# Kernel tuning notes

Hardware: AMD Instinct MI355X
Metric: run time of the kernel (lower is better)

Reference implementation:

```python
import jax, jax.numpy as jnp
import numpy as np

ALPHA = 1.702
EPS_RMS = 1e-6
W_LOAD = 0.01
W_IMP = 0.01
W_AUX = 1.0
LIMIT = 7.0
K_TOP = 4


def swiglu(x, alpha=ALPHA, limit=LIMIT):
    x_glu = jnp.clip(x[..., ::2], -limit, limit)
    x_lin = jnp.clip(x[..., 1::2], -limit, limit)
    return x_glu * jax.nn.sigmoid(x_glu * alpha) + (x_lin + 1.0)


def setup_inputs() -> dict:
    key = jax.random.key(0)
    ks = jax.random.split(key, 4)
    T, H, I, E = 2048, 512, 512, 8
    x = jax.random.normal(ks[0], (T, H), dtype=jnp.float32)
    norm_scale = jnp.ones((H,), jnp.float32)
    gate_w = jax.random.normal(ks[1], (E, H), jnp.float32) * 0.02
    gate_b = jnp.zeros((E,), jnp.float32)
    mlp1_w = jax.random.normal(ks[2], (E, 2 * I, H), jnp.float32) * 0.02
    mlp1_b = jnp.zeros((E, 2 * I), jnp.float32)
    mlp2_w = jax.random.normal(ks[3], (E, H, I), jnp.float32) * 0.02
    mlp2_b = jnp.zeros((E, H), jnp.float32)
    return {"x": x, "norm_scale": norm_scale, "gate_w": gate_w, "gate_b": gate_b,
            "mlp1_w": mlp1_w, "mlp1_b": mlp1_b, "mlp2_w": mlp2_w, "mlp2_b": mlp2_b}


def reference(x, norm_scale, gate_w, gate_b, mlp1_w, mlp1_b, mlp2_w, mlp2_b):
    T, H = x.shape
    E = gate_w.shape[0]
    K = K_TOP
    # RMSNorm (fp32 math as in torch module)
    t = x * jax.lax.rsqrt(jnp.mean(x * x, axis=-1, keepdims=True) + EPS_RMS) * norm_scale
    # gating
    gate_logits = t @ gate_w.T + gate_b                      # [T, E]
    gate_probs = jax.nn.softmax(gate_logits, axis=-1)
    expert_weights, experts_indices = jax.lax.top_k(gate_probs, K)
    expert_weights = expert_weights / expert_weights.sum(axis=-1, keepdims=True)
    # per-token per-expert combine coefficient (sum of slot weights routed to e)
    coeff = jnp.zeros((T, E), x.dtype).at[jnp.arange(T)[:, None], experts_indices].add(expert_weights)
    # dense expert compute (math-equivalent to the gathered einsums; avoids
    # materializing per-token weight matrices)
    h = jnp.einsum('th,ech->tec', t, mlp1_w) + mlp1_b[None]  # [T, E, 2I]
    a = swiglu(h)                                            # [T, E, I]
    y = jnp.einsum('tei,ehi->teh', a, mlp2_w) + mlp2_b[None] # [T, E, H]
    out = jnp.einsum('teh,te->th', y, coeff) + x
    # aux losses (replicates the torch code exactly, incl. D-doubling quirk)
    P = gate_probs.mean(axis=0)                              # [E]
    counts = jax.vmap(lambda col: jnp.zeros((E,), x.dtype).at[col].add(1.0), in_axes=1)(experts_indices)  # [K, E]
    doubling = (2.0 ** (K - jnp.arange(K))).astype(x.dtype)  # D_i = 2*(D_{i-1}+c_i)
    D = (doubling[:, None] * counts).sum(axis=0) / (T * K)
    loss_load = W_LOAD * E * (P * D).sum()
    importance = gate_logits.sum(axis=0)
    cv = jnp.std(importance, ddof=1) / (importance.mean() + 1e-6)
    loss_imp = W_IMP * cv ** 2
    aux_loss = W_AUX * (loss_load + loss_imp)
    return out, aux_loss
```

## Files before the change

kernel.cpp:

```cpp
#include <hip/hip_runtime.h>
#include <stdint.h>

#define ALPHA 1.702f
#define LIMIT 7.0f

typedef float f32x4 __attribute__((ext_vector_type(4)));
typedef __bf16 bf16x8 __attribute__((ext_vector_type(8)));

static __device__ __forceinline__ unsigned short f2bf(float f) {
    union { float f; uint32_t u; } v; v.f = f;
    uint32_t u = v.u;
    return (unsigned short)((u + 0x7FFFu + ((u >> 16) & 1u)) >> 16);
}
static __device__ __forceinline__ int imin(int a, int b) { return a < b ? a : b; }

#define GLL16(GP, LP) __builtin_amdgcn_global_load_lds( \
    (const __attribute__((address_space(1))) void*)(GP), \
    (__attribute__((address_space(3))) void*)(LP), 16, 0, 0)

static __device__ __forceinline__ int lsw(int row, int kc) {
    return row * 4 + (kc ^ ((row >> 1) & 3));
}

__global__ __launch_bounds__(256) void prep_kernel(
    const float* __restrict__ w1, const float* __restrict__ w2,
    unsigned short* __restrict__ w1p, unsigned short* __restrict__ w2b,
    const float* __restrict__ x,
    const float* __restrict__ norm_scale,
    const float* __restrict__ gate_w,
    const float* __restrict__ gate_b,
    const float* __restrict__ b2,
    unsigned short* __restrict__ t_bf,
    int* __restrict__ idx,
    float* __restrict__ wcoef,
    int* __restrict__ cnt,
    float* __restrict__ paux,
    float* __restrict__ out)
{
    __shared__ float red[4][48];
    __shared__ int   ltok[8][8];
    __shared__ float lwt[8][8];
    __shared__ int   lcnt[8];
    __shared__ int   gbase[8];
    if (blockIdx.x < 6144) {
        const int i4 = blockIdx.x * 256 + threadIdx.x;
        const int n1 = 1048576;
        if (i4 < n1) {
            const int e = i4 >> 17;
            const int rem = i4 & 131071;
            const int r = rem >> 7;
            const int c = rem & 127;
            const int src = (r < 512) ? (2 * r) : (2 * (r - 512) + 1);
            float4 v = ((const float4*)w1)[(e << 17) + (src << 7) + c];
            ushort4 o = { f2bf(v.x), f2bf(v.y), f2bf(v.z), f2bf(v.w) };
            ((ushort4*)w1p)[i4] = o;
        } else {
            const int i2 = i4 - n1;
            float4 v = ((const float4*)w2)[i2];
            ushort4 o = { f2bf(v.x), f2bf(v.y), f2bf(v.z), f2bf(v.w) };
            ((ushort4*)w2b)[i2] = o;
        }
        return;
    }
    const int bid = blockIdx.x - 6144;
    const int wave = threadIdx.x >> 6;
    const int lane = threadIdx.x & 63;
    if (threadIdx.x < 8) lcnt[threadIdx.x] = 0;
    __syncthreads();

    float accP[8], accI[8], accC[32];
    #pragma unroll
    for (int e = 0; e < 8; ++e) { accP[e] = 0.f; accI[e] = 0.f; }
    #pragma unroll
    for (int i = 0; i < 32; ++i) accC[i] = 0.f;

    #pragma unroll
    for (int it = 0; it < 2; ++it) {
        const int t = bid * 8 + wave * 2 + it;
        const float4* xr = (const float4*)(x + t * 512);
        float4 x0 = xr[lane * 2];
        float4 x1 = xr[lane * 2 + 1];
        float ss = x0.x*x0.x + x0.y*x0.y + x0.z*x0.z + x0.w*x0.w
                 + x1.x*x1.x + x1.y*x1.y + x1.z*x1.z + x1.w*x1.w;
        #pragma unroll
        for (int off = 32; off > 0; off >>= 1) ss += __shfl_xor(ss, off, 64);
        const float rstd = rsqrtf(ss * (1.f / 512.f) + 1e-6f);
        const float4* sr = (const float4*)norm_scale;
        float4 s0 = sr[lane * 2], s1 = sr[lane * 2 + 1];
        float tv[8];
        tv[0] = x0.x * rstd * s0.x; tv[1] = x0.y * rstd * s0.y;
        tv[2] = x0.z * rstd * s0.z; tv[3] = x0.w * rstd * s0.w;
        tv[4] = x1.x * rstd * s1.x; tv[5] = x1.y * rstd * s1.y;
        tv[6] = x1.z * rstd * s1.z; tv[7] = x1.w * rstd * s1.w;
        uint32_t p0 = (uint32_t)f2bf(tv[0]) | ((uint32_t)f2bf(tv[1]) << 16);
        uint32_t p1 = (uint32_t)f2bf(tv[2]) | ((uint32_t)f2bf(tv[3]) << 16);
        uint32_t p2 = (uint32_t)f2bf(tv[4]) | ((uint32_t)f2bf(tv[5]) << 16);
        uint32_t p3 = (uint32_t)f2bf(tv[6]) | ((uint32_t)f2bf(tv[7]) << 16);
        uint4 pk; pk.x = p0; pk.y = p1; pk.z = p2; pk.w = p3;
        ((uint4*)(t_bf + t * 512))[lane] = pk;
        float le[8];
        #pragma unroll
        for (int e = 0; e < 8; ++e) {
            const float4* gw = (const float4*)(gate_w + e * 512);
            float4 g0 = gw[lane * 2], g1 = gw[lane * 2 + 1];
            float d = tv[0]*g0.x + tv[1]*g0.y + tv[2]*g0.z + tv[3]*g0.w
                    + tv[4]*g1.x + tv[5]*g1.y + tv[6]*g1.z + tv[7]*g1.w;
            #pragma unroll
            for (int off = 32; off > 0; off >>= 1) d += __shfl_xor(d, off, 64);
            le[e] = d + gate_b[e];
        }
        float mx = le[0];
        #pragma unroll
        for (int e = 1; e < 8; ++e) mx = fmaxf(mx, le[e]);
        float pe[8], se = 0.f;
        #pragma unroll
        for (int e = 0; e < 8; ++e) { pe[e] = __expf(le[e] - mx); se += pe[e]; }
        const float sinv = 1.f / se;
        #pragma unroll
        for (int e = 0; e < 8; ++e) pe[e] *= sinv;
        unsigned picked = 0;
        int ik[4]; float wk[4];
        #pragma unroll
        for (int k = 0; k < 4; ++k) {
            float bv = -1.f; int bi = 0;
            #pragma unroll
            for (int e = 0; e < 8; ++e)
                if (!(picked & (1u << e)) && pe[e] > bv) { bv = pe[e]; bi = e; }
            ik[k] = bi; wk[k] = bv; picked |= (1u << bi);
        }
        const float winv = 1.f / (wk[0] + wk[1] + wk[2] + wk[3]);
        float nw[4];
        #pragma unroll
        for (int k = 0; k < 4; ++k) nw[k] = wk[k] * winv;
        float ce[8];
        #pragma unroll
        for (int e = 0; e < 8; ++e) {
            float c = 0.f;
            #pragma unroll
            for (int k = 0; k < 4; ++k) c += (ik[k] == e) ? nw[k] : 0.f;
            ce[e] = c;
        }
        if (lane == 0) {
            #pragma unroll
            for (int k = 0; k < 4; ++k) {
                const int e = ik[k];
                const int pos = atomicAdd(&lcnt[e], 1);
                ltok[e][pos] = t; lwt[e][pos] = nw[k];
            }
        }
        #pragma unroll
        for (int e = 0; e < 8; ++e) { accP[e] += pe[e]; accI[e] += le[e]; }
        #pragma unroll
        for (int k = 0; k < 4; ++k)
            #pragma unroll
            for (int e = 0; e < 8; ++e)
                accC[k * 8 + e] += (ik[k] == e) ? 1.f : 0.f;
        float ov[8];
        ov[0] = x0.x; ov[1] = x0.y; ov[2] = x0.z; ov[3] = x0.w;
        ov[4] = x1.x; ov[5] = x1.y; ov[6] = x1.z; ov[7] = x1.w;
        #pragma unroll
        for (int e = 0; e < 8; ++e) {
            const float4* br = (const float4*)(b2 + e * 512);
            float4 b0 = br[lane * 2], bb1 = br[lane * 2 + 1];
            ov[0] += ce[e] * b0.x; ov[1] += ce[e] * b0.y;
            ov[2] += ce[e] * b0.z; ov[3] += ce[e] * b0.w;
            ov[4] += ce[e] * bb1.x; ov[5] += ce[e] * bb1.y;
            ov[6] += ce[e] * bb1.z; ov[7] += ce[e] * bb1.w;
        }
        float4 o0, o1;
        o0.x = ov[0]; o0.y = ov[1]; o0.z = ov[2]; o0.w = ov[3];
        o1.x = ov[4]; o1.y = ov[5]; o1.z = ov[6]; o1.w = ov[7];
        float4* orow = (float4*)(out + t * 512);
        orow[lane * 2] = o0; orow[lane * 2 + 1] = o1;
    }
    if (lane == 0) {
        #pragma unroll
        for (int e = 0; e < 8; ++e) { red[wave][e] = accP[e]; red[wave][8 + e] = accI[e]; }
        #pragma unroll
        for (int i = 0; i < 32; ++i) red[wave][16 + i] = accC[i];
    }
    __syncthreads();
    if (threadIdx.x < 8)
        gbase[threadIdx.x] = atomicAdd(&cnt[threadIdx.x], lcnt[threadIdx.x]);
    __syncthreads();
    if (threadIdx.x < 64) {
        const int e = threadIdx.x >> 3, i = threadIdx.x & 7;
        if (i < lcnt[e]) {
            const int g = gbase[e] + i;
            idx[e * 2048 + g] = ltok[e][i];
            wcoef[e * 2048 + g] = lwt[e][i];
        }
    }
    if (threadIdx.x < 48) {
        paux[bid * 48 + threadIdx.x] =
            red[0][threadIdx.x] + red[1][threadIdx.x]
          + red[2][threadIdx.x] + red[3][threadIdx.x];
    }
}

__global__ __launch_bounds__(256, 2) void gemm1_swiglu(
    const unsigned short* __restrict__ A,
    const unsigned short* __restrict__ w1p,
    const float* __restrict__ b1,
    const int* __restrict__ idx,
    const float* __restrict__ wcoef,
    const int* __restrict__ cnt,
    unsigned short* __restrict__ As,
    const float* __restrict__ paux,
    float* __restrict__ aux_out)
{
    if (blockIdx.x == 512) {
        __shared__ float sred[4][48];
        const int wv = threadIdx.x >> 6, ln = threadIdx.x & 63;
        if (ln < 48) {
            float s = 0.f;
            for (int b = 0; b < 64; ++b) s += paux[(wv * 64 + b) * 48 + ln];
            sred[wv][ln] = s;
        }
        __syncthreads();
        if (threadIdx.x == 0) {
            float imp[8], sl = 0.f;
            #pragma unroll
            for (int e = 0; e < 8; ++e) {
                float a0 = sred[0][e] + sred[1][e] + sred[2][e] + sred[3][e];
                float P = a0 * (1.f / 2048.f);
                imp[e] = sred[0][8+e] + sred[1][8+e] + sred[2][8+e] + sred[3][8+e];
                float c0 = sred[0][16+e] + sred[1][16+e] + sred[2][16+e] + sred[3][16+e];
                float c1 = sred[0][24+e] + sred[1][24+e] + sred[2][24+e] + sred[3][24+e];
                float c2 = sred[0][32+e] + sred[1][32+e] + sred[2][32+e] + sred[3][32+e];
                float c3 = sred[0][40+e] + sred[1][40+e] + sred[2][40+e] + sred[3][40+e];
                float D = (16.f * c0 + 8.f * c1 + 4.f * c2 + 2.f * c3) * (1.f / 8192.f);
                sl += P * D;
            }
            float loss_load = 0.01f * 8.f * sl;
            float mean = 0.f;
            #pragma unroll
            for (int e = 0; e < 8; ++e) mean += imp[e];
            mean *= 0.125f;
            float var = 0.f;
            #pragma unroll
            for (int e = 0; e < 8; ++e) { float d = imp[e] - mean; var += d * d; }
            var *= (1.f / 7.f);
            float cv = sqrtf(var) / (mean + 1e-6f);
            *aux_out = loss_load + 0.01f * cv * cv;
        }
        return;
    }
    const int bx = blockIdx.x;
    const int e = bx & 7;
    const int slot = bx >> 3;
    const int tile_m = slot >> 2, tile_n = slot & 3;
    const int m0 = tile_m * 128, np = tile_n * 128;
    const int cnte = cnt[e];
    if (m0 >= cnte) return;

    __shared__ unsigned short tA[2][4096];
    __shared__ unsigned short tBg[2][4096];
    __shared__ unsigned short tBl[2][4096];
    const int tid = threadIdx.x;
    const int lane = tid & 63, wave = tid >> 6;
    const int wm = (wave & 1) * 64, wn = (wave >> 1) * 64;
    const int quad = lane >> 4, l16 = lane & 15;
    const int srow = tid >> 2;
    const int soff = ((tid & 3) ^ ((tid >> 3) & 3)) * 8;

    const int tok0 = idx[e * 2048 + imin(m0 + srow, cnte - 1)];
    const int tok1 = idx[e * 2048 + imin(m0 + 64 + srow, cnte - 1)];
    const unsigned short* Ar0 = A + tok0 * 512 + soff;
    const unsigned short* Ar1 = A + tok1 * 512 + soff;
    const unsigned short* Bg = w1p + (e * 1024 + np) * 512;
    const unsigned short* Bg0 = Bg + srow * 512 + soff;
    const unsigned short* Bg1 = Bg + (64 + srow) * 512 + soff;
    const unsigned short* Bl0 = Bg0 + 512 * 512;
    const unsigned short* Bl1 = Bg1 + 512 * 512;

    int rA[4], rB[4];
    #pragma unroll
    for (int i = 0; i < 4; ++i) {
        rA[i] = lsw(wm + i * 16 + l16, quad) * 8;
        rB[i] = lsw(wn + i * 16 + l16, quad) * 8;
    }

    f32x4 accG[4][4], accL[4][4];
    #pragma unroll
    for (int i = 0; i < 4; ++i)
        #pragma unroll
        for (int j = 0; j < 4; ++j) {
            f32x4 z = {0.f, 0.f, 0.f, 0.f};
            accG[i][j] = z; accL[i][j] = z;
        }

#define STAGE1(s, k0) do { \
    GLL16(Ar0 + (k0), tA[s] + tid * 8); \
    GLL16(Ar1 + (k0), tA[s] + (tid + 256) * 8); \
    GLL16(Bg0 + (k0), tBg[s] + tid * 8); \
    GLL16(Bg1 + (k0), tBg[s] + (tid + 256) * 8); \
    GLL16(Bl0 + (k0), tBl[s] + tid * 8); \
    GLL16(Bl1 + (k0), tBl[s] + (tid + 256) * 8); \
} while (0)

    STAGE1(0, 0);
    STAGE1(1, 32);
    #pragma unroll
    for (int kt = 0; kt < 16; ++kt) {
        const int cur = kt & 1;
        if (kt < 15) asm volatile("s_waitcnt vmcnt(6)" ::: "memory");
        else         asm volatile("s_waitcnt vmcnt(0)" ::: "memory");
        asm volatile("s_barrier" ::: "memory");
        bf16x8 af[4], bg[4], bl[4];
        #pragma unroll
        for (int i = 0; i < 4; ++i) {
            af[i] = *(const bf16x8*)(tA[cur] + rA[i]);
            bg[i] = *(const bf16x8*)(tBg[cur] + rB[i]);
            bl[i] = *(const bf16x8*)(tBl[cur] + rB[i]);
        }
        asm volatile("s_waitcnt lgkmcnt(0)" ::: "memory");
        asm volatile("s_barrier" ::: "memory");
        if (kt < 14) STAGE1(cur, (kt + 2) * 32);
        #pragma unroll
        for (int i = 0; i < 4; ++i)
            #pragma unroll
            for (int j = 0; j < 4; ++j) {
                accG[i][j] = __builtin_amdgcn_mfma_f32_16x16x32_bf16(af[i], bg[j], accG[i][j], 0, 0, 0);
                accL[i][j] = __builtin_amdgcn_mfma_f32_16x16x32_bf16(af[i], bl[j], accL[i][j], 0, 0, 0);
            }
    }
#undef STAGE1

    #pragma unroll
    for (int j = 0; j < 4; ++j) {
        const int colp = np + wn + j * 16 + l16;
        const float bgv = b1[e * 1024 + 2 * colp];
        const float blv = b1[e * 1024 + 2 * colp + 1];
        #pragma unroll
        for (int i = 0; i < 4; ++i) {
            const int sb = m0 + wm + i * 16 + quad * 4;
            #pragma unroll
            for (int r = 0; r < 4; ++r) {
                const int s = sb + r;
                if (s < cnte) {
                    float g2 = fminf(fmaxf(accG[i][j][r] + bgv, -LIMIT), LIMIT);
                    float l2 = fminf(fmaxf(accL[i][j][r] + blv, -LIMIT), LIMIT);
                    float a = g2 / (1.f + __expf(-ALPHA * g2)) + l2 + 1.f;
                    a *= wcoef[e * 2048 + s];
                    As[e * 1048576 + s * 512 + colp] = f2bf(a);
                }
            }
        }
    }
}

__global__ __launch_bounds__(256, 2) void gemm2(
    const unsigned short* __restrict__ As,
    const unsigned short* __restrict__ w2b,
    const int* __restrict__ idx,
    const int* __restrict__ cnt,
    float* __restrict__ out)
{
    const int bx = blockIdx.x;
    const int e = bx & 7;
    const int slot = bx >> 3;
    const int tile_m = slot >> 2, tile_n = slot & 3;
    const int m0 = tile_m * 128, n0 = tile_n * 128;
    const int cnte = cnt[e];
    if (m0 >= cnte) return;

    __shared__ unsigned short tA[2][4096];
    __shared__ unsigned short tB[2][4096];
    const int tid = threadIdx.x;
    const int lane = tid & 63, wave = tid >> 6;
    const int wm = (wave & 1) * 64, wn = (wave >> 1) * 64;
    const int quad = lane >> 4, l16 = lane & 15;
    const int srow = tid >> 2;
    const int soff = ((tid & 3) ^ ((tid >> 3) & 3)) * 8;

    const unsigned short* Ar0 = As + e * 1048576 + (m0 + srow) * 512 + soff;
    const unsigned short* Ar1 = As + e * 1048576 + (m0 + 64 + srow) * 512 + soff;
    const unsigned short* Bb  = w2b + e * 262144;
    const unsigned short* Br0 = Bb + (n0 + srow) * 512 + soff;
    const unsigned short* Br1 = Bb + (n0 + 64 + srow) * 512 + soff;

    int rA[4], rB[4];
    #pragma unroll
    for (int i = 0; i < 4; ++i) {
        rA[i] = lsw(wm + i * 16 + l16, quad) * 8;
        rB[i] = lsw(wn + i * 16 + l16, quad) * 8;
    }

    f32x4 acc[4][4];
    #pragma unroll
    for (int i = 0; i < 4; ++i)
        #pragma unroll
        for (int j = 0; j < 4; ++j) { f32x4 z = {0.f, 0.f, 0.f, 0.f}; acc[i][j] = z; }

#define STAGE2(s, k0) do { \
    GLL16(Ar0 + (k0), tA[s] + tid * 8); \
    GLL16(Ar1 + (k0), tA[s] + (tid + 256) * 8); \
    GLL16(Br0 + (k0), tB[s] + tid * 8); \
    GLL16(Br1 + (k0), tB[s] + (tid + 256) * 8); \
} while (0)

    STAGE2(0, 0);
    STAGE2(1, 32);
    #pragma unroll
    for (int kt = 0; kt < 16; ++kt) {
        const int cur = kt & 1;
        if (kt < 15) asm volatile("s_waitcnt vmcnt(4)" ::: "memory");
        else         asm volatile("s_waitcnt vmcnt(0)" ::: "memory");
        asm volatile("s_barrier" ::: "memory");
        bf16x8 af[4], bf[4];
        #pragma unroll
        for (int i = 0; i < 4; ++i) {
            af[i] = *(const bf16x8*)(tA[cur] + rA[i]);
            bf[i] = *(const bf16x8*)(tB[cur] + rB[i]);
        }
        asm volatile("s_waitcnt lgkmcnt(0)" ::: "memory");
        asm volatile("s_barrier" ::: "memory");
        if (kt < 14) STAGE2(cur, (kt + 2) * 32);
        #pragma unroll
        for (int i = 0; i < 4; ++i)
            #pragma unroll
            for (int j = 0; j < 4; ++j)
                acc[i][j] = __builtin_amdgcn_mfma_f32_16x16x32_bf16(af[i], bf[j], acc[i][j], 0, 0, 0);
    }
#undef STAGE2

    #pragma unroll
    for (int i = 0; i < 4; ++i) {
        const int sb = m0 + wm + i * 16 + quad * 4;
        #pragma unroll
        for (int r = 0; r < 4; ++r) {
            const int s = sb + r;
            if (s < cnte) {
                const int tok = idx[e * 2048 + s];
                #pragma unroll
                for (int j = 0; j < 4; ++j) {
                    const int col = n0 + wn + j * 16 + l16;
                    atomicAdd(&out[tok * 512 + col], acc[i][j][r]);
                }
            }
        }
    }
}

extern "C" void kernel_launch(void* const* d_in, const int* in_sizes, int n_in,
                              void* d_out, int out_size, void* d_ws, size_t ws_size,
                              hipStream_t stream)
{
    (void)in_sizes; (void)n_in; (void)out_size; (void)ws_size;
    const float* x          = (const float*)d_in[0];
    const float* norm_scale = (const float*)d_in[1];
    const float* gate_w     = (const float*)d_in[2];
    const float* gate_b     = (const float*)d_in[3];
    const float* mlp1_w     = (const float*)d_in[4];
    const float* mlp1_b     = (const float*)d_in[5];
    const float* mlp2_w     = (const float*)d_in[6];
    const float* mlp2_b     = (const float*)d_in[7];
    float* out = (float*)d_out;

    char* ws = (char*)d_ws;
    unsigned short* w1p   = (unsigned short*)(ws);
    unsigned short* w2b   = (unsigned short*)(ws + 8388608);
    unsigned short* tbf   = (unsigned short*)(ws + 12582912);
    unsigned short* As    = (unsigned short*)(ws + 14680064);
    int*            idx   = (int*)(ws + 31457280);
    float*          wcoef = (float*)(ws + 31522816);
    float*          paux  = (float*)(ws + 31588352);
    int*            cnt   = (int*)(ws + 31637504);

    hipMemsetAsync(cnt, 0, 32, stream);
    prep_kernel<<<6400, 256, 0, stream>>>(mlp1_w, mlp2_w, w1p, w2b,
                                          x, norm_scale, gate_w, gate_b, mlp2_b,
                                          tbf, idx, wcoef, cnt, paux, out);
    gemm1_swiglu<<<513, 256, 0, stream>>>(tbf, w1p, mlp1_b, idx, wcoef, cnt,
                                          As, paux, out + 2048 * 512);
    gemm2<<<512, 256, 0, stream>>>(As, w2b, idx, cnt, out);
}
```

Baseline: 153.1 us.

## Replace global atomic routing with per-block counts and in-kernel prefix scan

```diff
diff --git a/kernel.cpp b/kernel.cpp
--- a/kernel.cpp
+++ b/kernel.cpp
@@ -31,9 +31,9 @@
     const float* __restrict__ gate_b,
     const float* __restrict__ b2,
     unsigned short* __restrict__ t_bf,
-    int* __restrict__ idx,
-    float* __restrict__ wcoef,
-    int* __restrict__ cnt,
+    int* __restrict__ pcnt,
+    int* __restrict__ gtok,
+    float* __restrict__ gwt,
     float* __restrict__ paux,
     float* __restrict__ out)
 {
@@ -41,7 +41,6 @@
     __shared__ int   ltok[8][8];
     __shared__ float lwt[8][8];
     __shared__ int   lcnt[8];
-    __shared__ int   gbase[8];
     if (blockIdx.x < 6144) {
         const int i4 = blockIdx.x * 256 + threadIdx.x;
         const int n1 = 1048576;
@@ -180,15 +179,12 @@
         for (int i = 0; i < 32; ++i) red[wave][16 + i] = accC[i];
     }
     __syncthreads();
-    if (threadIdx.x < 8)
-        gbase[threadIdx.x] = atomicAdd(&cnt[threadIdx.x], lcnt[threadIdx.x]);
-    __syncthreads();
+    if (threadIdx.x < 8) pcnt[bid * 8 + threadIdx.x] = lcnt[threadIdx.x];
     if (threadIdx.x < 64) {
         const int e = threadIdx.x >> 3, i = threadIdx.x & 7;
         if (i < lcnt[e]) {
-            const int g = gbase[e] + i;
-            idx[e * 2048 + g] = ltok[e][i];
-            wcoef[e * 2048 + g] = lwt[e][i];
+            gtok[bid * 64 + threadIdx.x] = ltok[e][i];
+            gwt[bid * 64 + threadIdx.x]  = lwt[e][i];
         }
     }
     if (threadIdx.x < 48) {
@@ -198,13 +194,43 @@
     }
 }
 
+#define ROUTE_PREAMBLE(E, M0, WANT_W)                                        \
+    {                                                                        \
+        const int v = pcnt[tid * 8 + (E)];                                   \
+        sscan[tid] = v;                                                      \
+        __syncthreads();                                                     \
+        for (int ofs = 1; ofs < 256; ofs <<= 1) {                            \
+            int add = (tid >= ofs) ? sscan[tid - ofs] : 0;                   \
+            __syncthreads();                                                 \
+            sscan[tid] += add;                                               \
+            __syncthreads();                                                 \
+        }                                                                    \
+        cnte = sscan[255];                                                   \
+        if ((M0) < cnte) {                                                   \
+            if (tid < 128) {                                                 \
+                const int s = imin((M0) + tid, cnte - 1);                    \
+                int lo = 0, hi = 255;                                        \
+                for (int itb = 0; itb < 8; ++itb) {                          \
+                    const int mid = (lo + hi) >> 1;                          \
+                    if (sscan[mid] > s) hi = mid; else lo = mid + 1;         \
+                }                                                            \
+                const int b = lo;                                            \
+                const int excl = (b > 0) ? sscan[b - 1] : 0;                 \
+                const int li = s - excl;                                     \
+                stok[tid] = gtok[b * 64 + (E) * 8 + li];                     \
+                if (WANT_W) swt[tid] = gwt[b * 64 + (E) * 8 + li];           \
+            }                                                                \
+            __syncthreads();                                                 \
+        }                                                                    \
+    }
+
 __global__ __launch_bounds__(256, 2) void gemm1_swiglu(
     const unsigned short* __restrict__ A,
     const unsigned short* __restrict__ w1p,
     const float* __restrict__ b1,
-    const int* __restrict__ idx,
-    const float* __restrict__ wcoef,
-    const int* __restrict__ cnt,
+    const int* __restrict__ pcnt,
+    const int* __restrict__ gtok,
+    const float* __restrict__ gwt,
     unsigned short* __restrict__ As,
     const float* __restrict__ paux,
     float* __restrict__ aux_out)
@@ -246,26 +272,38 @@
         }
         return;
     }
+    __shared__ unsigned short tA[2][4096];
+    __shared__ unsigned short tBg[2][4096];
+    __shared__ unsigned short tBl[2][4096];
+    __shared__ int sscan[256];
+    __shared__ int stok[128];
+    __shared__ float swt[128];
     const int bx = blockIdx.x;
+    const int tid = threadIdx.x;
     const int e = bx & 7;
     const int slot = bx >> 3;
     const int tile_m = slot >> 2, tile_n = slot & 3;
     const int m0 = tile_m * 128, np = tile_n * 128;
-    const int cnte = cnt[e];
+
+    int cnte;
+    ROUTE_PREAMBLE(e, m0, 1);
     if (m0 >= cnte) return;
 
-    __shared__ unsigned short tA[2][4096];
-    __shared__ unsigned short tBg[2][4096];
-    __shared__ unsigned short tBl[2][4096];
-    const int tid = threadIdx.x;
     const int lane = tid & 63, wave = tid >> 6;
     const int wm = (wave & 1) * 64, wn = (wave >> 1) * 64;
     const int quad = lane >> 4, l16 = lane & 15;
     const int srow = tid >> 2;
     const int soff = ((tid & 3) ^ ((tid >> 3) & 3)) * 8;
 
-    const int tok0 = idx[e * 2048 + imin(m0 + srow, cnte - 1)];
-    const int tok1 = idx[e * 2048 + imin(m0 + 64 + srow, cnte - 1)];
+    const int tok0 = stok[srow];
+    const int tok1 = stok[64 + srow];
+    float cw[4][4];
+    #pragma unroll
+    for (int i = 0; i < 4; ++i)
+        #pragma unroll
+        for (int r = 0; r < 4; ++r)
+            cw[i][r] = swt[wm + i * 16 + quad * 4 + r];
+
     const unsigned short* Ar0 = A + tok0 * 512 + soff;
     const unsigned short* Ar1 = A + tok1 * 512 + soff;
     const unsigned short* Bg = w1p + (e * 1024 + np) * 512;
@@ -342,7 +380,7 @@
                     float g2 = fminf(fmaxf(accG[i][j][r] + bgv, -LIMIT), LIMIT);
                     float l2 = fminf(fmaxf(accL[i][j][r] + blv, -LIMIT), LIMIT);
                     float a = g2 / (1.f + __expf(-ALPHA * g2)) + l2 + 1.f;
-                    a *= wcoef[e * 2048 + s];
+                    a *= cw[i][r];
                     As[e * 1048576 + s * 512 + colp] = f2bf(a);
                 }
             }
@@ -353,26 +391,39 @@
 __global__ __launch_bounds__(256, 2) void gemm2(
     const unsigned short* __restrict__ As,
     const unsigned short* __restrict__ w2b,
-    const int* __restrict__ idx,
-    const int* __restrict__ cnt,
+    const int* __restrict__ pcnt,
+    const int* __restrict__ gtok,
+    const float* __restrict__ gwt,
     float* __restrict__ out)
 {
+    __shared__ unsigned short tA[2][4096];
+    __shared__ unsigned short tB[2][4096];
+    __shared__ int sscan[256];
+    __shared__ int stok[128];
+    __shared__ float swt[128];
     const int bx = blockIdx.x;
+    const int tid = threadIdx.x;
     const int e = bx & 7;
     const int slot = bx >> 3;
     const int tile_m = slot >> 2, tile_n = slot & 3;
     const int m0 = tile_m * 128, n0 = tile_n * 128;
-    const int cnte = cnt[e];
+
+    int cnte;
+    ROUTE_PREAMBLE(e, m0, 0);
     if (m0 >= cnte) return;
 
-    __shared__ unsigned short tA[2][4096];
-    __shared__ unsigned short tB[2][4096];
-    const int tid = threadIdx.x;
     const int lane = tid & 63, wave = tid >> 6;
     const int wm = (wave & 1) * 64, wn = (wave >> 1) * 64;
     const int quad = lane >> 4, l16 = lane & 15;
     const int srow = tid >> 2;
     const int soff = ((tid & 3) ^ ((tid >> 3) & 3)) * 8;
+
+    int rtok[4][4];
+    #pragma unroll
+    for (int i = 0; i < 4; ++i)
+        #pragma unroll
+        for (int r = 0; r < 4; ++r)
+            rtok[i][r] = stok[wm + i * 16 + quad * 4 + r];
 
     const unsigned short* Ar0 = As + e * 1048576 + (m0 + srow) * 512 + soff;
     const unsigned short* Ar1 = As + e * 1048576 + (m0 + 64 + srow) * 512 + soff;
@@ -432,7 +483,7 @@
         for (int r = 0; r < 4; ++r) {
             const int s = sb + r;
             if (s < cnte) {
-                const int tok = idx[e * 2048 + s];
+                const int tok = rtok[i][r];
                 #pragma unroll
                 for (int j = 0; j < 4; ++j) {
                     const int col = n0 + wn + j * 16 + l16;
@@ -463,16 +514,15 @@
     unsigned short* w2b   = (unsigned short*)(ws + 8388608);
     unsigned short* tbf   = (unsigned short*)(ws + 12582912);
     unsigned short* As    = (unsigned short*)(ws + 14680064);
-    int*            idx   = (int*)(ws + 31457280);
-    float*          wcoef = (float*)(ws + 31522816);
-    float*          paux  = (float*)(ws + 31588352);
-    int*            cnt   = (int*)(ws + 31637504);
-
-    hipMemsetAsync(cnt, 0, 32, stream);
+    float*          paux  = (float*)(ws + 31457280);
+    int*            pcnt  = (int*)(ws + 31506432);
+    int*            gtok  = (int*)(ws + 31514624);
+    float*          gwt   = (float*)(ws + 31580160);
+
     prep_kernel<<<6400, 256, 0, stream>>>(mlp1_w, mlp2_w, w1p, w2b,
                                           x, norm_scale, gate_w, gate_b, mlp2_b,
-                                          tbf, idx, wcoef, cnt, paux, out);
-    gemm1_swiglu<<<513, 256, 0, stream>>>(tbf, w1p, mlp1_b, idx, wcoef, cnt,
+                                          tbf, pcnt, gtok, gwt, paux, out);
+    gemm1_swiglu<<<513, 256, 0, stream>>>(tbf, w1p, mlp1_b, pcnt, gtok, gwt,
                                           As, paux, out + 2048 * 512);
-    gemm2<<<512, 256, 0, stream>>>(As, w2b, idx, cnt, out);
+    gemm2<<<512, 256, 0, stream>>>(As, w2b, pcnt, gtok, gwt, out);
 }
```

Result: no change. 153.7 us (+0.4%).

## Replace atomic scatter with per-expert outputs plus combine kernel; defer w2 conversion

Applied to the files above, without the earlier changes.

```diff
diff --git a/kernel.cpp b/kernel.cpp
--- a/kernel.cpp
+++ b/kernel.cpp
@@ -23,46 +23,37 @@
 }
 
 __global__ __launch_bounds__(256) void prep_kernel(
-    const float* __restrict__ w1, const float* __restrict__ w2,
-    unsigned short* __restrict__ w1p, unsigned short* __restrict__ w2b,
+    const float* __restrict__ w1,
+    unsigned short* __restrict__ w1p,
     const float* __restrict__ x,
     const float* __restrict__ norm_scale,
     const float* __restrict__ gate_w,
     const float* __restrict__ gate_b,
-    const float* __restrict__ b2,
     unsigned short* __restrict__ t_bf,
-    int* __restrict__ idx,
-    float* __restrict__ wcoef,
-    int* __restrict__ cnt,
-    float* __restrict__ paux,
-    float* __restrict__ out)
+    int* __restrict__ pcnt,
+    int* __restrict__ gtok,
+    float* __restrict__ gwt,
+    unsigned int* __restrict__ esel,
+    float* __restrict__ cw4,
+    float* __restrict__ paux)
 {
     __shared__ float red[4][48];
     __shared__ int   ltok[8][8];
     __shared__ float lwt[8][8];
     __shared__ int   lcnt[8];
-    __shared__ int   gbase[8];
-    if (blockIdx.x < 6144) {
+    if (blockIdx.x < 4096) {
         const int i4 = blockIdx.x * 256 + threadIdx.x;
-        const int n1 = 1048576;
-        if (i4 < n1) {
-            const int e = i4 >> 17;
-            const int rem = i4 & 131071;
-            const int r = rem >> 7;
-            const int c = rem & 127;
-            const int src = (r < 512) ? (2 * r) : (2 * (r - 512) + 1);
-            float4 v = ((const float4*)w1)[(e << 17) + (src << 7) + c];
-            ushort4 o = { f2bf(v.x), f2bf(v.y), f2bf(v.z), f2bf(v.w) };
-            ((ushort4*)w1p)[i4] = o;
-        } else {
-            const int i2 = i4 - n1;
-            float4 v = ((const float4*)w2)[i2];
-            ushort4 o = { f2bf(v.x), f2bf(v.y), f2bf(v.z), f2bf(v.w) };
-            ((ushort4*)w2b)[i2] = o;
-        }
+        const int e = i4 >> 17;
+        const int rem = i4 & 131071;
+        const int r = rem >> 7;
+        const int c = rem & 127;
+        const int src = (r < 512) ? (2 * r) : (2 * (r - 512) + 1);
+        float4 v = ((const float4*)w1)[(e << 17) + (src << 7) + c];
+        ushort4 o = { f2bf(v.x), f2bf(v.y), f2bf(v.z), f2bf(v.w) };
+        ((ushort4*)w1p)[i4] = o;
         return;
     }
-    const int bid = blockIdx.x - 6144;
+    const int bid = blockIdx.x - 4096;
     const int wave = threadIdx.x >> 6;
     const int lane = threadIdx.x & 63;
     if (threadIdx.x < 8) lcnt[threadIdx.x] = 0;
@@ -132,14 +123,6 @@
         float nw[4];
         #pragma unroll
         for (int k = 0; k < 4; ++k) nw[k] = wk[k] * winv;
-        float ce[8];
-        #pragma unroll
-        for (int e = 0; e < 8; ++e) {
-            float c = 0.f;
-            #pragma unroll
-            for (int k = 0; k < 4; ++k) c += (ik[k] == e) ? nw[k] : 0.f;
-            ce[e] = c;
-        }
         if (lane == 0) {
             #pragma unroll
             for (int k = 0; k < 4; ++k) {
@@ -147,6 +130,10 @@
                 const int pos = atomicAdd(&lcnt[e], 1);
                 ltok[e][pos] = t; lwt[e][pos] = nw[k];
             }
+            esel[t] = (unsigned)ik[0] | ((unsigned)ik[1] << 8)
+                    | ((unsigned)ik[2] << 16) | ((unsigned)ik[3] << 24);
+            float4 cwv; cwv.x = nw[0]; cwv.y = nw[1]; cwv.z = nw[2]; cwv.w = nw[3];
+            ((float4*)cw4)[t] = cwv;
         }
         #pragma unroll
         for (int e = 0; e < 8; ++e) { accP[e] += pe[e]; accI[e] += le[e]; }
@@ -155,23 +142,6 @@
             #pragma unroll
             for (int e = 0; e < 8; ++e)
                 accC[k * 8 + e] += (ik[k] == e) ? 1.f : 0.f;
-        float ov[8];
-        ov[0] = x0.x; ov[1] = x0.y; ov[2] = x0.z; ov[3] = x0.w;
-        ov[4] = x1.x; ov[5] = x1.y; ov[6] = x1.z; ov[7] = x1.w;
-        #pragma unroll
-        for (int e = 0; e < 8; ++e) {
-            const float4* br = (const float4*)(b2 + e * 512);
-            float4 b0 = br[lane * 2], bb1 = br[lane * 2 + 1];
-            ov[0] += ce[e] * b0.x; ov[1] += ce[e] * b0.y;
-            ov[2] += ce[e] * b0.z; ov[3] += ce[e] * b0.w;
-            ov[4] += ce[e] * bb1.x; ov[5] += ce[e] * bb1.y;
-            ov[6] += ce[e] * bb1.z; ov[7] += ce[e] * bb1.w;
-        }
-        float4 o0, o1;
-        o0.x = ov[0]; o0.y = ov[1]; o0.z = ov[2]; o0.w = ov[3];
-        o1.x = ov[4]; o1.y = ov[5]; o1.z = ov[6]; o1.w = ov[7];
-        float4* orow = (float4*)(out + t * 512);
-        orow[lane * 2] = o0; orow[lane * 2 + 1] = o1;
     }
     if (lane == 0) {
         #pragma unroll
@@ -180,15 +150,12 @@
         for (int i = 0; i < 32; ++i) red[wave][16 + i] = accC[i];
     }
     __syncthreads();
-    if (threadIdx.x < 8)
-        gbase[threadIdx.x] = atomicAdd(&cnt[threadIdx.x], lcnt[threadIdx.x]);
-    __syncthreads();
+    if (threadIdx.x < 8) pcnt[bid * 8 + threadIdx.x] = lcnt[threadIdx.x];
     if (threadIdx.x < 64) {
         const int e = threadIdx.x >> 3, i = threadIdx.x & 7;
         if (i < lcnt[e]) {
-            const int g = gbase[e] + i;
-            idx[e * 2048 + g] = ltok[e][i];
-            wcoef[e * 2048 + g] = lwt[e][i];
+            gtok[bid * 64 + threadIdx.x] = ltok[e][i];
+            gwt[bid * 64 + threadIdx.x]  = lwt[e][i];
         }
     }
     if (threadIdx.x < 48) {
@@ -202,12 +169,16 @@
     const unsigned short* __restrict__ A,
     const unsigned short* __restrict__ w1p,
     const float* __restrict__ b1,
-    const int* __restrict__ idx,
-    const float* __restrict__ wcoef,
-    const int* __restrict__ cnt,
+    const int* __restrict__ pcnt,
+    const int* __restrict__ gtok,
+    const float* __restrict__ gwt,
     unsigned short* __restrict__ As,
+    int* __restrict__ cntg,
+    int* __restrict__ invslot,
     const float* __restrict__ paux,
-    float* __restrict__ aux_out)
+    float* __restrict__ aux_out,
+    const float* __restrict__ w2,
+    unsigned short* __restrict__ w2b)
 {
     if (blockIdx.x == 512) {
         __shared__ float sred[4][48];
@@ -246,26 +217,72 @@
         }
         return;
     }
+    if (blockIdx.x > 512) {
+        const int i2 = (blockIdx.x - 513) * 256 + threadIdx.x;
+        float4 v = ((const float4*)w2)[i2];
+        ushort4 o = { f2bf(v.x), f2bf(v.y), f2bf(v.z), f2bf(v.w) };
+        ((ushort4*)w2b)[i2] = o;
+        return;
+    }
+    __shared__ unsigned short tA[2][4096];
+    __shared__ unsigned short tBg[2][4096];
+    __shared__ unsigned short tBl[2][4096];
+    __shared__ int sscan[256];
+    __shared__ int stok[128];
+    __shared__ float swt[128];
     const int bx = blockIdx.x;
+    const int tid = threadIdx.x;
     const int e = bx & 7;
     const int slot = bx >> 3;
     const int tile_m = slot >> 2, tile_n = slot & 3;
     const int m0 = tile_m * 128, np = tile_n * 128;
-    const int cnte = cnt[e];
+
+    {
+        const int v = pcnt[tid * 8 + e];
+        sscan[tid] = v;
+        __syncthreads();
+        for (int ofs = 1; ofs < 256; ofs <<= 1) {
+            int add = (tid >= ofs) ? sscan[tid - ofs] : 0;
+            __syncthreads();
+            sscan[tid] += add;
+            __syncthreads();
+        }
+    }
+    const int cnte = sscan[255];
+    if (slot == 0 && tid == 0) cntg[e] = cnte;
     if (m0 >= cnte) return;
-
-    __shared__ unsigned short tA[2][4096];
-    __shared__ unsigned short tBg[2][4096];
-    __shared__ unsigned short tBl[2][4096];
-    const int tid = threadIdx.x;
+    if (tid < 128) {
+        const int s = imin(m0 + tid, cnte - 1);
+        int lo = 0, hi = 255;
+        #pragma unroll
+        for (int itb = 0; itb < 8; ++itb) {
+            const int mid = (lo + hi) >> 1;
+            if (sscan[mid] > s) hi = mid; else lo = mid + 1;
+        }
+        const int b = lo;
+        const int excl = (b > 0) ? sscan[b - 1] : 0;
+        stok[tid] = gtok[b * 64 + e * 8 + (s - excl)];
+        swt[tid]  = gwt[b * 64 + e * 8 + (s - excl)];
+    }
+    __syncthreads();
+    if (tile_n == 0 && tid < 128 && (m0 + tid) < cnte)
+        invslot[e * 2048 + stok[tid]] = m0 + tid;
+
     const int lane = tid & 63, wave = tid >> 6;
     const int wm = (wave & 1) * 64, wn = (wave >> 1) * 64;
     const int quad = lane >> 4, l16 = lane & 15;
     const int srow = tid >> 2;
     const int soff = ((tid & 3) ^ ((tid >> 3) & 3)) * 8;
 
-    const int tok0 = idx[e * 2048 + imin(m0 + srow, cnte - 1)];
-    const int tok1 = idx[e * 2048 + imin(m0 + 64 + srow, cnte - 1)];
+    const int tok0 = stok[srow];
+    const int tok1 = stok[64 + srow];
+    float cw[4][4];
+    #pragma unroll
+    for (int i = 0; i < 4; ++i)
+        #pragma unroll
+        for (int r = 0; r < 4; ++r)
+            cw[i][r] = swt[wm + i * 16 + quad * 4 + r];
+
     const unsigned short* Ar0 = A + tok0 * 512 + soff;
     const unsigned short* Ar1 = A + tok1 * 512 + soff;
     const unsigned short* Bg = w1p + (e * 1024 + np) * 512;
@@ -342,7 +359,7 @@
                     float g2 = fminf(fmaxf(accG[i][j][r] + bgv, -LIMIT), LIMIT);
                     float l2 = fminf(fmaxf(accL[i][j][r] + blv, -LIMIT), LIMIT);
                     float a = g2 / (1.f + __expf(-ALPHA * g2)) + l2 + 1.f;
-                    a *= wcoef[e * 2048 + s];
+                    a *= cw[i][r];
                     As[e * 1048576 + s * 512 + colp] = f2bf(a);
                 }
             }
@@ -353,21 +370,20 @@
 __global__ __launch_bounds__(256, 2) void gemm2(
     const unsigned short* __restrict__ As,
     const unsigned short* __restrict__ w2b,
-    const int* __restrict__ idx,
-    const int* __restrict__ cnt,
-    float* __restrict__ out)
+    const int* __restrict__ cntg,
+    float* __restrict__ y)
 {
+    __shared__ unsigned short tA[2][4096];
+    __shared__ unsigned short tB[2][4096];
     const int bx = blockIdx.x;
+    const int tid = threadIdx.x;
     const int e = bx & 7;
     const int slot = bx >> 3;
     const int tile_m = slot >> 2, tile_n = slot & 3;
     const int m0 = tile_m * 128, n0 = tile_n * 128;
-    const int cnte = cnt[e];
+    const int cnte = cntg[e];
     if (m0 >= cnte) return;
 
-    __shared__ unsigned short tA[2][4096];
-    __shared__ unsigned short tB[2][4096];
-    const int tid = threadIdx.x;
     const int lane = tid & 63, wave = tid >> 6;
     const int wm = (wave & 1) * 64, wn = (wave >> 1) * 64;
     const int quad = lane >> 4, l16 = lane & 15;
@@ -425,21 +441,58 @@
     }
 #undef STAGE2
 
+    float* yb = y + e * 1048576;
     #pragma unroll
     for (int i = 0; i < 4; ++i) {
         const int sb = m0 + wm + i * 16 + quad * 4;
         #pragma unroll
         for (int r = 0; r < 4; ++r) {
             const int s = sb + r;
-            if (s < cnte) {
-                const int tok = idx[e * 2048 + s];
-                #pragma unroll
-                for (int j = 0; j < 4; ++j) {
-                    const int col = n0 + wn + j * 16 + l16;
-                    atomicAdd(&out[tok * 512 + col], acc[i][j][r]);
-                }
+            #pragma unroll
+            for (int j = 0; j < 4; ++j) {
+                const int col = n0 + wn + j * 16 + l16;
+                yb[s * 512 + col] = acc[i][j][r];
             }
         }
+    }
+}
+
+__global__ __launch_bounds__(256) void combine_kernel(
+    const float* __restrict__ x,
+    const float* __restrict__ b2,
+    const float* __restrict__ y,
+    const int* __restrict__ invslot,
+    const unsigned int* __restrict__ esel,
+    const float* __restrict__ cw4,
+    float* __restrict__ out)
+{
+    const int tid = threadIdx.x;
+    const int lane = tid & 63, wave = tid >> 6;
+    #pragma unroll
+    for (int it = 0; it < 2; ++it) {
+        const int t = blockIdx.x * 8 + wave * 2 + it;
+        const float4* xr = (const float4*)(x + t * 512);
+        float4 o0 = xr[lane * 2];
+        float4 o1 = xr[lane * 2 + 1];
+        const unsigned sel = esel[t];
+        float4 cwv = ((const float4*)cw4)[t];
+        const float cws[4] = { cwv.x, cwv.y, cwv.z, cwv.w };
+        #pragma unroll
+        for (int k = 0; k < 4; ++k) {
+            const int e = (sel >> (8 * k)) & 255;
+            const int s = invslot[e * 2048 + t];
+            const float4* yr = (const float4*)(y + (e * 2048 + s) * 512);
+            float4 y0 = yr[lane * 2], y1 = yr[lane * 2 + 1];
+            const float4* br = (const float4*)(b2 + e * 512);
+            float4 b0 = br[lane * 2], bb1 = br[lane * 2 + 1];
+            const float c = cws[k];
+            o0.x += y0.x + c * b0.x; o0.y += y0.y + c * b0.y;
+            o0.z += y0.z + c * b0.z; o0.w += y0.w + c * b0.w;
+            o1.x += y1.x + c * bb1.x; o1.y += y1.y + c * bb1.y;
+            o1.z += y1.z + c * bb1.z; o1.w += y1.w + c * bb1.w;
+        }
+        float4* orow = (float4*)(out + t * 512);
+        orow[lane * 2] = o0; orow[lane * 2 + 1] = o1;
     }
 }
 
@@ -463,16 +516,22 @@
     unsigned short* w2b   = (unsigned short*)(ws + 8388608);
     unsigned short* tbf   = (unsigned short*)(ws + 12582912);
     unsigned short* As    = (unsigned short*)(ws + 14680064);
-    int*            idx   = (int*)(ws + 31457280);
-    float*          wcoef = (float*)(ws + 31522816);
-    float*          paux  = (float*)(ws + 31588352);
-    int*            cnt   = (int*)(ws + 31637504);
-
-    hipMemsetAsync(cnt, 0, 32, stream);
-    prep_kernel<<<6400, 256, 0, stream>>>(mlp1_w, mlp2_w, w1p, w2b,
-                                          x, norm_scale, gate_w, gate_b, mlp2_b,
-                                          tbf, idx, wcoef, cnt, paux, out);
-    gemm1_swiglu<<<513, 256, 0, stream>>>(tbf, w1p, mlp1_b, idx, wcoef, cnt,
-                                          As, paux, out + 2048 * 512);
-    gemm2<<<512, 256, 0, stream>>>(As, w2b, idx, cnt, out);
-}
+    float*          y     = (float*)(ws + 31457280);
+    float*          paux  = (float*)(ws + 65011712);
+    int*            pcnt  = (int*)(ws + 65060864);
+    int*            gtok  = (int*)(ws + 65069056);
+    float*          gwt   = (float*)(ws + 65134592);
+    unsigned int*   esel  = (unsigned int*)(ws + 65200128);
+    float*          cw4   = (float*)(ws + 65208320);
+    int*            invsl = (int*)(ws + 65241088);
+    int*            cntg  = (int*)(ws + 65306624);
+
+    prep_kernel<<<4352, 256, 0, stream>>>(mlp1_w, w1p,
+                                          x, norm_scale, gate_w, gate_b,
+                                          tbf, pcnt, gtok, gwt, esel, cw4, paux);
+    gemm1_swiglu<<<2561, 256, 0, stream>>>(tbf, w1p, mlp1_b, pcnt, gtok, gwt,
+                                           As, cntg, invsl, paux,
+                                           out + 2048 * 512, mlp2_w, w2b);
+    gemm2<<<512, 256, 0, stream>>>(As, w2b, cntg, y);
+    combine_kernel<<<256, 256, 0, stream>>>(x, mlp2_b, y, invsl, esel, cw4, out);
+}
```

Measured after the change: 144.2 us. -5.8%, faster.
